# Kernel optimization log

Measured on AMD Instinct MI355X. Metric: run time of the kernel, lower is better.

The kernel has to match this reference:

```python
import jax, jax.numpy as jnp
import numpy as np

D_MODEL = 1024
N_HEADS = 16
HEAD_DIM = D_MODEL // N_HEADS
N_EXPERTS = 4
HIDDEN = 4 * D_MODEL
B, T = 1, 2048


def _apply_rope(x, sin, cos):
    # x: [..., D]; sin/cos broadcastable to [..., D/2]
    x1, x2 = x[..., ::2], x[..., 1::2]
    r1 = x1 * cos - x2 * sin
    r2 = x1 * sin + x2 * cos
    return jnp.stack((r1, r2), axis=-1).reshape(x.shape)


def setup_inputs() -> dict:
    key = jax.random.key(0)
    ks = jax.random.split(key, 16)
    s = 0.02
    d, E, Hd = D_MODEL, N_EXPERTS, HIDDEN
    return {
        "x": jax.random.normal(ks[0], (B, T, d), dtype=jnp.float32),
        "w_dw": jax.random.normal(ks[1], (d, 3), dtype=jnp.float32) * s,      # depthwise conv k=3
        "w_pw": jax.random.normal(ks[2], (d, d), dtype=jnp.float32) * s,      # pointwise conv [out,in]
        "w_qkv": jax.random.normal(ks[3], (3 * d, d), dtype=jnp.float32) * s,  # [out,in]
        "w_o": jax.random.normal(ks[4], (d, d), dtype=jnp.float32) * s,
        "w_gate": jax.random.normal(ks[5], (d, d), dtype=jnp.float32) * s,
        "b_gate": jnp.zeros((d,), dtype=jnp.float32),
        "ln_g": jnp.ones((d,), dtype=jnp.float32),
        "ln_b": jnp.zeros((d,), dtype=jnp.float32),
        "w_moe_gate": jax.random.normal(ks[6], (E, d), dtype=jnp.float32) * s,  # Linear no bias [out,in]
        "w1": jax.random.normal(ks[7], (E, Hd, d), dtype=jnp.float32) * s,
        "b1": jnp.zeros((E, Hd), dtype=jnp.float32),
        "w2": jax.random.normal(ks[8], (E, d, Hd), dtype=jnp.float32) * s,
        "b2": jnp.zeros((E, d), dtype=jnp.float32),
    }


def reference(x, w_dw, w_pw, w_qkv, w_o, w_gate, b_gate, ln_g, ln_b,
              w_moe_gate, w1, b1, w2, b2):
    Bv, Tv, d = x.shape
    H, Dh = N_HEADS, HEAD_DIM
    dt = x.dtype

    # --- causal conv mixer (depthwise k=3, causal left pad 2, then pointwise) ---
    xp = jnp.pad(x, ((0, 0), (2, 0), (0, 0)))
    y = (xp[:, 0:Tv] * w_dw[:, 0] + xp[:, 1:Tv + 1] * w_dw[:, 1]
         + xp[:, 2:Tv + 2] * w_dw[:, 2])
    y = jnp.einsum('btd,ed->bte', y, w_pw)
    x = x + y

    # --- qkv projection + split heads ---
    qkv = jnp.einsum('btd,ed->bte', x, w_qkv).reshape(Bv, Tv, 3, H, Dh)
    q, k, v = qkv[:, :, 0], qkv[:, :, 1], qkv[:, :, 2]

    # --- RoPE (head_dim even) ---
    inv_freq = 1.0 / (10000.0 ** (jnp.arange(0, Dh, 2, dtype=dt) / Dh))
    pos = jnp.arange(Tv, dtype=dt)
    theta = pos[:, None] * inv_freq[None, :]                 # [T, Dh/2]
    sin = jnp.sin(theta)[None, :, None, :]                   # [1,T,1,Dh/2]
    cos = jnp.cos(theta)[None, :, None, :]
    q = _apply_rope(q, sin, cos)
    k = _apply_rope(k, sin, cos)

    # --- linear attention via full kv outer-product cumsum ---
    q_phi = jax.nn.elu(q) + 1.0
    k_phi = jax.nn.elu(k) + 1.0
    kv = k_phi[..., :, None] * v[..., None, :]               # [B,T,H,D,D]
    kv_prefix = jnp.cumsum(kv, axis=1)
    k_prefix = jnp.cumsum(k_phi, axis=1)
    num = jnp.einsum('bthd,bthdm->bthm', q_phi, kv_prefix)
    denom = jnp.sum(q_phi * k_prefix, axis=-1, keepdims=True)
    attn = num / (denom + 1e-6)
    attn = attn.reshape(Bv, Tv, d)
    attn = jnp.einsum('btd,ed->bte', attn, w_o)

    # --- delta-gated residual (dropout = identity in eval) ---
    delta = x - jnp.concatenate([x[:, :1], x[:, :-1]], axis=1)
    gate = jax.nn.sigmoid(jnp.einsum('btd,ed->bte', delta, w_gate) + b_gate)
    x = x + gate * attn

    # --- LayerNorm + dense MoE FFN ---
    mu = jnp.mean(x, axis=-1, keepdims=True)
    var = jnp.mean((x - mu) ** 2, axis=-1, keepdims=True)
    h = (x - mu) / jnp.sqrt(var + 1e-5) * ln_g + ln_b

    gw = jax.nn.softmax(jnp.einsum('btd,ed->bte', h, w_moe_gate), axis=-1)  # [B,T,E]
    hid = jax.nn.silu(jnp.einsum('btd,efd->btef', h, w1) + b1)              # [B,T,E,Hd]
    eo = jnp.einsum('btef,edf->bted', hid, w2) + b2                          # [B,T,E,d]
    ffn = jnp.einsum('bte,bted->btd', gw, eo)
    return x + ffn
```

## Files before the change

### kernel.cpp

```cpp
#include <hip/hip_runtime.h>
#include <hip/hip_bf16.h>

#define TSEQ 2048
#define DM   1024
#define NHD  16
#define DHD  64
#define NEXP 4
#define HIDN 4096
#define NMOE (NEXP*HIDN)
#define CHK  128
#define NCHK (TSEQ/CHK)

typedef __attribute__((ext_vector_type(8))) short          bf16x8_v;
typedef __attribute__((ext_vector_type(4))) float          f32x4_v;
typedef __attribute__((ext_vector_type(4))) unsigned short us4_v;

__device__ __forceinline__ unsigned short bfbits(float f) {
  __hip_bfloat16 h = __float2bfloat16(f);
  return __builtin_bit_cast(unsigned short, h);
}
__device__ __forceinline__ float bf2f(unsigned short u) {
  return __uint_as_float(((unsigned)u) << 16);
}
__device__ __forceinline__ float wave_sum(float v) {
  #pragma unroll
  for (int o = 32; o; o >>= 1) v += __shfl_xor(v, o, 64);
  return v;
}
__device__ __forceinline__ void gl_lds16(const void* g, void* l) {
  __builtin_amdgcn_global_load_lds((const __attribute__((address_space(1))) void*)g,
                                   (__attribute__((address_space(3))) void*)l, 16, 0, 0);
}

__global__ __launch_bounds__(256) void cvt_bf16(const float* __restrict__ in,
                                                unsigned short* __restrict__ out, int n4) {
  int i = blockIdx.x * 256 + threadIdx.x;
  if (i >= n4) return;
  float4 v = ((const float4*)in)[i];
  us4_v o; o.x = bfbits(v.x); o.y = bfbits(v.y); o.z = bfbits(v.z); o.w = bfbits(v.w);
  ((us4_v*)out)[i] = o;
}

__global__ __launch_bounds__(256) void perm_w2(const float* __restrict__ in,
                                               unsigned short* __restrict__ out) {
  int i = blockIdx.x * 256 + threadIdx.x;
  int i4 = i * 4;
  int f = i4 & (HIDN - 1);
  int r = i4 >> 12;
  int e = r >> 10, dd = r & 1023;
  float4 v = *(const float4*)&in[(size_t)r * HIDN + f];
  us4_v o; o.x = bfbits(v.x); o.y = bfbits(v.y); o.z = bfbits(v.z); o.w = bfbits(v.w);
  *(us4_v*)&out[(size_t)dd * NMOE + e * HIDN + f] = o;
}

__global__ __launch_bounds__(256) void conv_dw(const float* __restrict__ x,
                                               const float* __restrict__ w_dw,
                                               unsigned short* __restrict__ y_bf) {
  int i = blockIdx.x * 256 + threadIdx.x;
  int c = i & (DM - 1);
  int t = i >> 10;
  float a = (t >= 2) ? x[i - 2 * DM] : 0.f;
  float b = (t >= 1) ? x[i - DM]     : 0.f;
  float d = x[i];
  float y = a * w_dw[c * 3] + b * w_dw[c * 3 + 1] + d * w_dw[c * 3 + 2];
  y_bf[i] = bfbits(y);
}

template <int EPI>
__global__ __launch_bounds__(256) void gemm_bt(
    const unsigned short* __restrict__ A,  const unsigned short* __restrict__ A2,
    const unsigned short* __restrict__ B,  const unsigned short* __restrict__ B2,
    float* __restrict__ Cf, float* __restrict__ Cf2,
    unsigned short* __restrict__ Cbf,
    const float* __restrict__ ex0, const float* __restrict__ ex1,
    int lda, int ldb, int K, int ldc, int kPerZ)
{
  if (EPI == 0) { if (blockIdx.z) { A = A2; B = B2; Cf = Cf2; } }
  if (EPI == 3) { int ko = blockIdx.z * kPerZ; A += ko; B += ko; }

  __shared__ unsigned short As[2][128][32];
  __shared__ unsigned short Bs[2][128][32];

  const int tid = threadIdx.x;
  const int m0 = blockIdx.x << 7, n0 = blockIdx.y << 7;
  const int sr = tid >> 2, sc = (tid & 3) << 3;
  const unsigned short* gA = A + (size_t)(m0 + sr) * lda + sc;
  const unsigned short* gB = B + (size_t)(n0 + sr) * ldb + sc;

  const int lane = tid & 63, wv = tid >> 6;
  const int wr = (wv >> 1) << 6, wc = (wv & 1) << 6;
  const int fr = lane & 15, fk = (lane >> 4) << 3, r4 = (lane >> 4) << 2;

  f32x4_v acc[4][4] = {};

  auto stage = [&](int k0, int b) {
    gl_lds16(gA + k0,                     &As[b][sr][sc]);
    gl_lds16(gA + k0 + (size_t)64 * lda,  &As[b][sr + 64][sc]);
    gl_lds16(gB + k0,                     &Bs[b][sr][sc]);
    gl_lds16(gB + k0 + (size_t)64 * ldb,  &Bs[b][sr + 64][sc]);
  };

  stage(0, 0);
  __syncthreads();
  int cur = 0;
  for (int k0 = 0; k0 < K; k0 += 32) {
    if (k0 + 32 < K) stage(k0 + 32, cur ^ 1);
    bf16x8_v af[4], bfm[4];
    #pragma unroll
    for (int m = 0; m < 4; m++) af[m]  = *(const bf16x8_v*)&As[cur][wr + m * 16 + fr][fk];
    #pragma unroll
    for (int n = 0; n < 4; n++) bfm[n] = *(const bf16x8_v*)&Bs[cur][wc + n * 16 + fr][fk];
    #pragma unroll
    for (int m = 0; m < 4; m++)
      #pragma unroll
      for (int n = 0; n < 4; n++)
        acc[m][n] = __builtin_amdgcn_mfma_f32_16x16x32_bf16(af[m], bfm[n], acc[m][n], 0, 0, 0);
    __syncthreads();
    cur ^= 1;
  }

  #pragma unroll
  for (int m = 0; m < 4; m++) {
    #pragma unroll
    for (int n = 0; n < 4; n++) {
      #pragma unroll
      for (int j = 0; j < 4; j++) {
        int gr = m0 + wr + m * 16 + r4 + j;
        int gc = n0 + wc + n * 16 + fr;
        float v = acc[m][n][j];
        size_t off = (size_t)gr * ldc + gc;
        if (EPI == 0) {
          Cf[off] = v;
        } else if (EPI == 1) {
          float s = v + ex0[off];
          Cf[off] = s; Cbf[off] = bfbits(s);
        } else if (EPI == 2) {
          float c2 = v + ex0[gc];
          float sl = c2 / (1.f + __expf(-c2));
          Cbf[off] = bfbits(sl * ex1[gr * 4 + (gc >> 12)]);
        } else {
          atomicAdd(&Cf[off], v);
        }
      }
    }
  }
}

__global__ __launch_bounds__(256) void rope_phi(const float* __restrict__ qkv,
                                                unsigned short* __restrict__ qphi,
                                                unsigned short* __restrict__ kphi,
                                                unsigned short* __restrict__ vout) {
  int idx = blockIdx.x * 256 + threadIdx.x;
  int i = idx & 31;
  int h = (idx >> 5) & 15;
  int t = idx >> 9;
  const float* row = qkv + (size_t)t * 3 * DM;
  int col = h * 64 + 2 * i;
  float q0 = row[col],          q1 = row[col + 1];
  float k0 = row[DM + col],     k1 = row[DM + col + 1];
  float v0 = row[2 * DM + col], v1 = row[2 * DM + col + 1];
  float invf = __expf(-(float)(2 * i) * (9.210340371976184f / 64.f));
  float th = (float)t * invf;
  float s, c;
  sincosf(th, &s, &c);
  float qr0 = q0 * c - q1 * s, qr1 = q0 * s + q1 * c;
  float kr0 = k0 * c - k1 * s, kr1 = k0 * s + k1 * c;
  size_t o = (size_t)t * DM + col;
  qphi[o]     = bfbits(qr0 > 0.f ? qr0 + 1.f : __expf(qr0));
  qphi[o + 1] = bfbits(qr1 > 0.f ? qr1 + 1.f : __expf(qr1));
  kphi[o]     = bfbits(kr0 > 0.f ? kr0 + 1.f : __expf(kr0));
  kphi[o + 1] = bfbits(kr1 > 0.f ? kr1 + 1.f : __expf(kr1));
  vout[o]     = bfbits(v0);
  vout[o + 1] = bfbits(v1);
}

__global__ __launch_bounds__(256) void kv_chunk(const unsigned short* __restrict__ kphi,
                                                const unsigned short* __restrict__ vbf,
                                                float* __restrict__ kvT,
                                                float* __restrict__ ksbuf) {
  int h = blockIdx.x & 15, c = blockIdx.x >> 4;
  __shared__ unsigned short Kt[64][136];
  __shared__ unsigned short Vt[64][136];
  int tid = threadIdx.x;
  int rr = tid >> 3, cc = (tid & 7) << 3;
  int t0 = c * CHK;
  #pragma unroll
  for (int g = 0; g < 4; g++) {
    int t = g * 32 + rr;
    bf16x8_v k8 = *(const bf16x8_v*)&kphi[(size_t)(t0 + t) * DM + h * 64 + cc];
    bf16x8_v v8 = *(const bf16x8_v*)&vbf [(size_t)(t0 + t) * DM + h * 64 + cc];
    #pragma unroll
    for (int j = 0; j < 8; j++) { Kt[cc + j][t] = (unsigned short)k8[j];
                                  Vt[cc + j][t] = (unsigned short)v8[j]; }
  }
  __syncthreads();
  int lane = tid & 63, wv = tid >> 6;
  int wr = (wv >> 1) << 5, wc = (wv & 1) << 5;
  int fr = lane & 15, fk = (lane >> 4) << 3, r4 = (lane >> 4) << 2;
  f32x4_v acc[2][2] = {};
  #pragma unroll
  for (int k0 = 0; k0 < 128; k0 += 32) {
    bf16x8_v a[2], b[2];
    #pragma unroll
    for (int m = 0; m < 2; m++) a[m] = *(const bf16x8_v*)&Kt[wr + m * 16 + fr][k0 + fk];
    #pragma unroll
    for (int n = 0; n < 2; n++) b[n] = *(const bf16x8_v*)&Vt[wc + n * 16 + fr][k0 + fk];
    #pragma unroll
    for (int m = 0; m < 2; m++)
      #pragma unroll
      for (int n = 0; n < 2; n++)
        acc[m][n] = __builtin_amdgcn_mfma_f32_16x16x32_bf16(a[m], b[n], acc[m][n], 0, 0, 0);
  }
  float* kvout = kvT + (size_t)(h * NCHK + c) * 4096;
  #pragma unroll
  for (int m = 0; m < 2; m++)
    #pragma unroll
    for (int n = 0; n < 2; n++)
      #pragma unroll
      for (int j = 0; j < 4; j++)
        kvout[(wc + n * 16 + fr) * 64 + (wr + m * 16 + r4 + j)] = acc[m][n][j];
  float s = 0.f;
  int d = tid >> 2, q = tid & 3;
  for (int i = 0; i < 32; i++) s += bf2f(Kt[d][q * 32 + i]);
  s += __shfl_xor(s, 1, 64); s += __shfl_xor(s, 2, 64);
  if (q == 0) ksbuf[(h * NCHK + c) * 64 + d] = s;
}

__global__ __launch_bounds__(256) void prefix_kv(const float* __restrict__ kvT,
                                                 const float* __restrict__ ksbuf,
                                                 unsigned short* __restrict__ sT,
                                                 float* __restrict__ kspre) {
  int idx = blockIdx.x * 256 + threadIdx.x;
  int h = idx >> 12, nd = idx & 4095;
  float s = 0.f;
  for (int c = 0; c < NCHK; c++) {
    size_t o = (size_t)(h * NCHK + c) * 4096 + nd;
    sT[o] = bfbits(s);
    s += kvT[o];
  }
  if (idx < NHD * 64) {
    float ks = 0.f;
    for (int c = 0; c < NCHK; c++) {
      int o = ((idx >> 6) * NCHK + c) * 64 + (idx & 63);
      kspre[o] = ks;
      ks += ksbuf[o];
    }
  }
}

__global__ __launch_bounds__(256) void attn_chunk(const unsigned short* __restrict__ qphi,
                                                  const unsigned short* __restrict__ kphi,
                                                  const unsigned short* __restrict__ vbf,
                                                  const unsigned short* __restrict__ sT,
                                                  const float* __restrict__ kspre,
                                                  float* __restrict__ num,
                                                  float* __restrict__ den) {
  int h = blockIdx.x & 15, c = blockIdx.x >> 4;
  __shared__ unsigned short Qs[128][72];
  __shared__ unsigned short Ks[128][72];
  __shared__ unsigned short Ms[128][200];
  __shared__ unsigned short Vt[64][200];
  __shared__ float ksL[64];
  int tid = threadIdx.x;
  int t0 = c * CHK;
  int rr = tid >> 3, cc = (tid & 7) << 3;
  #pragma unroll
  for (int g = 0; g < 4; g++) {
    int t = g * 32 + rr;
    bf16x8_v q8 = *(const bf16x8_v*)&qphi[(size_t)(t0 + t) * DM + h * 64 + cc];
    bf16x8_v k8 = *(const bf16x8_v*)&kphi[(size_t)(t0 + t) * DM + h * 64 + cc];
    bf16x8_v v8 = *(const bf16x8_v*)&vbf [(size_t)(t0 + t) * DM + h * 64 + cc];
    *(bf16x8_v*)&Qs[t][cc] = q8;
    *(bf16x8_v*)&Ks[t][cc] = k8;
    *(bf16x8_v*)&Ms[t][128 + cc] = q8;
    #pragma unroll
    for (int j = 0; j < 8; j++) Vt[cc + j][t] = (unsigned short)v8[j];
  }
  #pragma unroll
  for (int g = 0; g < 2; g++) {
    int e = (g * 256 + tid) * 8;
    bf16x8_v s8 = *(const bf16x8_v*)&sT[(size_t)(h * NCHK + c) * 4096 + e];
    *(bf16x8_v*)&Vt[e >> 6][128 + (e & 63)] = s8;
  }
  if (tid < 64) ksL[tid] = kspre[(h * NCHK + c) * 64 + tid];
  __syncthreads();

  int lane = tid & 63, wv = tid >> 6;
  int wr = (wv >> 1) << 6, wc = (wv & 1) << 6;
  int fr = lane & 15, fk = (lane >> 4) << 3, r4 = (lane >> 4) << 2;
  {
    f32x4_v acc[4][4] = {};
    #pragma unroll
    for (int k0 = 0; k0 < 64; k0 += 32) {
      bf16x8_v a[4], b[4];
      #pragma unroll
      for (int m = 0; m < 4; m++) a[m] = *(const bf16x8_v*)&Qs[wr + m * 16 + fr][k0 + fk];
      #pragma unroll
      for (int n = 0; n < 4; n++) b[n] = *(const bf16x8_v*)&Ks[wc + n * 16 + fr][k0 + fk];
      #pragma unroll
      for (int m = 0; m < 4; m++)
        #pragma unroll
        for (int n = 0; n < 4; n++)
          acc[m][n] = __builtin_amdgcn_mfma_f32_16x16x32_bf16(a[m], b[n], acc[m][n], 0, 0, 0);
    }
    #pragma unroll
    for (int m = 0; m < 4; m++)
      #pragma unroll
      for (int n = 0; n < 4; n++)
        #pragma unroll
        for (int j = 0; j < 4; j++) {
          int r = wr + m * 16 + r4 + j, col = wc + n * 16 + fr;
          Ms[r][col] = bfbits(col <= r ? acc[m][n][j] : 0.f);
        }
  }
  __syncthreads();
  {
    int dr = tid >> 1, half = tid & 1;
    float s = 0.f;
    for (int i = 0; i < 64; i++) s += bf2f(Ms[dr][half * 64 + i]);
    for (int i = 0; i < 32; i++) {
      int d = half * 32 + i;
      s += bf2f(Qs[dr][d]) * ksL[d];
    }
    s += __shfl_xor(s, 1, 64);
    if (!half) den[(size_t)(t0 + dr) * NHD + h] = s;
  }
  {
    int wc2 = (wv & 1) << 5;
    f32x4_v acc[4][2] = {};
    #pragma unroll
    for (int k0 = 0; k0 < 192; k0 += 32) {
      bf16x8_v a[4], b[2];
      #pragma unroll
      for (int m = 0; m < 4; m++) a[m] = *(const bf16x8_v*)&Ms[wr + m * 16 + fr][k0 + fk];
      #pragma unroll
      for (int n = 0; n < 2; n++) b[n] = *(const bf16x8_v*)&Vt[wc2 + n * 16 + fr][k0 + fk];
      #pragma unroll
      for (int m = 0; m < 4; m++)
        #pragma unroll
        for (int n = 0; n < 2; n++)
          acc[m][n] = __builtin_amdgcn_mfma_f32_16x16x32_bf16(a[m], b[n], acc[m][n], 0, 0, 0);
    }
    #pragma unroll
    for (int m = 0; m < 4; m++)
      #pragma unroll
      for (int n = 0; n < 2; n++)
        #pragma unroll
        for (int j = 0; j < 4; j++)
          num[(size_t)(t0 + wr + m * 16 + r4 + j) * DM + h * 64 + wc2 + n * 16 + fr]
              = acc[m][n][j];
  }
}

__global__ __launch_bounds__(256) void div_cvt(const float* __restrict__ attn_num,
                                               const float* __restrict__ denom,
                                               const float* __restrict__ x1,
                                               unsigned short* __restrict__ attn_bf,
                                               unsigned short* __restrict__ delta_bf) {
  int i = blockIdx.x * 256 + threadIdx.x;
  int i4 = i * 4;
  int t = i4 >> 10, c = i4 & 1023, h = c >> 6;
  float dn = 1.f / (denom[t * NHD + h] + 1e-6f);
  float4 nm = *(const float4*)&attn_num[i4];
  us4_v a; a.x = bfbits(nm.x * dn); a.y = bfbits(nm.y * dn);
           a.z = bfbits(nm.z * dn); a.w = bfbits(nm.w * dn);
  *(us4_v*)&attn_bf[i4] = a;
  float4 xv = *(const float4*)&x1[i4];
  float4 xp = t ? *(const float4*)&x1[i4 - DM] : xv;
  us4_v d; d.x = bfbits(xv.x - xp.x); d.y = bfbits(xv.y - xp.y);
           d.z = bfbits(xv.z - xp.z); d.w = bfbits(xv.w - xp.w);
  *(us4_v*)&delta_bf[i4] = d;
}

__global__ __launch_bounds__(256) void fuse_ln(const float* __restrict__ x1,
                                               const float* __restrict__ attn_o,
                                               const float* __restrict__ gate_lin,
                                               const float* __restrict__ b_gate,
                                               const float* __restrict__ ln_g,
                                               const float* __restrict__ ln_b,
                                               const float* __restrict__ w_moe,
                                               float* __restrict__ x2,
                                               unsigned short* __restrict__ h_bf,
                                               float* __restrict__ gw) {
  int t = blockIdx.x;
  int tid = threadIdx.x;
  __shared__ float hrow[DM];
  __shared__ float red[16];
  float vals[4], s = 0.f, s2 = 0.f;
  #pragma unroll
  for (int j = 0; j < 4; j++) {
    int c = tid + j * 256;
    size_t ix = (size_t)t * DM + c;
    float g = gate_lin[ix] + b_gate[c];
    float sig = 1.f / (1.f + __expf(-g));
    float xv = x1[ix] + sig * attn_o[ix];
    x2[ix] = xv; vals[j] = xv; s += xv; s2 += xv * xv;
  }
  s = wave_sum(s); s2 = wave_sum(s2);
  int wvi = tid >> 6, l = tid & 63;
  if (l == 0) { red[wvi] = s; red[4 + wvi] = s2; }
  __syncthreads();
  s  = red[0] + red[1] + red[2] + red[3];
  s2 = red[4] + red[5] + red[6] + red[7];
  float mu = s * (1.f / DM);
  float var = s2 * (1.f / DM) - mu * mu;
  float rstd = rsqrtf(var + 1e-5f);
  #pragma unroll
  for (int j = 0; j < 4; j++) {
    int c = tid + j * 256;
    size_t ix = (size_t)t * DM + c;
    float h = (vals[j] - mu) * rstd * ln_g[c] + ln_b[c];
    h_bf[ix] = bfbits(h); hrow[c] = h;
  }
  __syncthreads();
  float dot = 0.f;
  for (int i0 = l; i0 < DM; i0 += 64) dot += hrow[i0] * w_moe[wvi * DM + i0];
  dot = wave_sum(dot);
  if (l == 0) red[8 + wvi] = dot;
  __syncthreads();
  if (tid == 0) {
    float a0 = red[8], a1 = red[9], a2 = red[10], a3 = red[11];
    float mx = fmaxf(fmaxf(a0, a1), fmaxf(a2, a3));
    float e0 = __expf(a0 - mx), e1 = __expf(a1 - mx), e2 = __expf(a2 - mx), e3 = __expf(a3 - mx);
    float inv = 1.f / (e0 + e1 + e2 + e3);
    gw[t * 4 + 0] = e0 * inv; gw[t * 4 + 1] = e1 * inv;
    gw[t * 4 + 2] = e2 * inv; gw[t * 4 + 3] = e3 * inv;
  }
}

__global__ __launch_bounds__(256) void init_out(const float* __restrict__ x2,
                                                const float* __restrict__ gw,
                                                const float* __restrict__ b2,
                                                float* __restrict__ out) {
  int i = blockIdx.x * 256 + threadIdx.x;
  int i4 = i * 4;
  int t = i4 >> 10, c = i4 & 1023;
  const float* g = gw + t * 4;
  float4 o = *(const float4*)&x2[i4];
  #pragma unroll
  for (int e = 0; e < 4; e++) {
    float ge = g[e];
    float4 b = *(const float4*)&b2[e * DM + c];
    o.x += ge * b.x; o.y += ge * b.y; o.z += ge * b.z; o.w += ge * b.w;
  }
  *(float4*)&out[i4] = o;
}

extern "C" void kernel_launch(void* const* d_in, const int* in_sizes, int n_in,
                              void* d_out, int out_size, void* d_ws, size_t ws_size,
                              hipStream_t stream) {
  const float* x      = (const float*)d_in[0];
  const float* w_dw   = (const float*)d_in[1];
  const float* w_pw   = (const float*)d_in[2];
  const float* w_qkv  = (const float*)d_in[3];
  const float* w_o    = (const float*)d_in[4];
  const float* w_gate = (const float*)d_in[5];
  const float* b_gate = (const float*)d_in[6];
  const float* ln_g   = (const float*)d_in[7];
  const float* ln_b   = (const float*)d_in[8];
  const float* w_moe  = (const float*)d_in[9];
  const float* w1     = (const float*)d_in[10];
  const float* b1     = (const float*)d_in[11];
  const float* w2     = (const float*)d_in[12];
  const float* b2     = (const float*)d_in[13];
  float* out = (float*)d_out;

  char* ws = (char*)d_ws;
  size_t off = 0;
  auto alloc = [&](size_t bytes) -> char* {
    char* p = ws + off; off += (bytes + 255) & ~(size_t)255; return p;
  };
  unsigned short* w_pw_bf   = (unsigned short*)alloc((size_t)DM * DM * 2);
  unsigned short* w_qkv_bf  = (unsigned short*)alloc((size_t)3 * DM * DM * 2);
  unsigned short* w_o_bf    = (unsigned short*)alloc((size_t)DM * DM * 2);
  unsigned short* w_gate_bf = (unsigned short*)alloc((size_t)DM * DM * 2);
  unsigned short* w1_bf     = (unsigned short*)alloc((size_t)NMOE * DM * 2);
  unsigned short* w2c_bf    = (unsigned short*)alloc((size_t)DM * NMOE * 2);
  float*          x1        = (float*)alloc((size_t)TSEQ * DM * 4);
  unsigned short* x1_bf     = (unsigned short*)alloc((size_t)TSEQ * DM * 2);
  unsigned short* y_bf      = (unsigned short*)alloc((size_t)TSEQ * DM * 2);
  float*          denomb    = (float*)alloc((size_t)TSEQ * NHD * 4);
  float*          gwb       = (float*)alloc((size_t)TSEQ * NEXP * 4);
  float*          attn_o    = (float*)alloc((size_t)TSEQ * DM * 4);
  unsigned short* delta_bf  = (unsigned short*)alloc((size_t)TSEQ * DM * 2);
  float*          gate_lin  = (float*)alloc((size_t)TSEQ * DM * 4);
  float*          x2        = (float*)alloc((size_t)TSEQ * DM * 4);
  unsigned short* h_bf      = (unsigned short*)alloc((size_t)TSEQ * DM * 2);
  float*          kvT       = (float*)alloc((size_t)NHD * NCHK * 4096 * 4);
  unsigned short* sTb       = (unsigned short*)alloc((size_t)NHD * NCHK * 4096 * 2);
  float*          ksbuf     = (float*)alloc((size_t)NHD * NCHK * 64 * 4);
  float*          kspre     = (float*)alloc((size_t)NHD * NCHK * 64 * 4);
  char*           pool      = alloc((size_t)TSEQ * NMOE * 2);
  if (off > ws_size) return;

  float*          qkv      = (float*)pool;
  unsigned short* qphi     = (unsigned short*)(pool + (size_t)TSEQ * 3 * DM * 4);
  unsigned short* kphi     = qphi + (size_t)TSEQ * DM;
  unsigned short* vbf      = kphi + (size_t)TSEQ * DM;
  float*          attn_num = (float*)(vbf + (size_t)TSEQ * DM);
  unsigned short* attn_bf  = (unsigned short*)(attn_num + (size_t)TSEQ * DM);
  unsigned short* hids     = (unsigned short*)pool;

  cvt_bf16<<<1024,  256, 0, stream>>>(w_pw,   w_pw_bf,   DM * DM / 4);
  cvt_bf16<<<3072,  256, 0, stream>>>(w_qkv,  w_qkv_bf,  3 * DM * DM / 4);
  cvt_bf16<<<1024,  256, 0, stream>>>(w_o,    w_o_bf,    DM * DM / 4);
  cvt_bf16<<<1024,  256, 0, stream>>>(w_gate, w_gate_bf, DM * DM / 4);
  cvt_bf16<<<16384, 256, 0, stream>>>(w1,     w1_bf,     NMOE * DM / 4);
  perm_w2<<<16384, 256, 0, stream>>>(w2, w2c_bf);

  conv_dw<<<8192, 256, 0, stream>>>(x, w_dw, y_bf);
  gemm_bt<1><<<dim3(16, 8, 1), 256, 0, stream>>>(y_bf, nullptr, w_pw_bf, nullptr,
      x1, nullptr, x1_bf, x, nullptr, DM, DM, DM, DM, 0);

  gemm_bt<0><<<dim3(16, 24, 1), 256, 0, stream>>>(x1_bf, nullptr, w_qkv_bf, nullptr,
      qkv, nullptr, nullptr, nullptr, nullptr, DM, DM, DM, 3 * DM, 0);
  rope_phi<<<4096, 256, 0, stream>>>(qkv, qphi, kphi, vbf);

  kv_chunk<<<NHD * NCHK, 256, 0, stream>>>(kphi, vbf, kvT, ksbuf);
  prefix_kv<<<256, 256, 0, stream>>>(kvT, ksbuf, sTb, kspre);
  attn_chunk<<<NHD * NCHK, 256, 0, stream>>>(qphi, kphi, vbf, sTb, kspre,
                                             attn_num, denomb);
  div_cvt<<<2048, 256, 0, stream>>>(attn_num, denomb, x1, attn_bf, delta_bf);

  gemm_bt<0><<<dim3(16, 8, 2), 256, 0, stream>>>(attn_bf, delta_bf, w_o_bf, w_gate_bf,
      attn_o, gate_lin, nullptr, nullptr, nullptr, DM, DM, DM, DM, 0);

  fuse_ln<<<2048, 256, 0, stream>>>(x1, attn_o, gate_lin, b_gate, ln_g, ln_b, w_moe,
                                    x2, h_bf, gwb);

  init_out<<<2048, 256, 0, stream>>>(x2, gwb, b2, out);
  gemm_bt<2><<<dim3(16, 128, 1), 256, 0, stream>>>(h_bf, nullptr, w1_bf, nullptr,
      nullptr, nullptr, hids, b1, gwb, DM, DM, DM, NMOE, 0);
  gemm_bt<3><<<dim3(16, 8, 4), 256, 0, stream>>>(hids, nullptr, w2c_bf, nullptr,
      out, nullptr, nullptr, nullptr, nullptr, NMOE, NMOE, HIDN, DM, HIDN);
}
```

Baseline: 411.5 us.

## Add 256x256-tile GEMM kernel for the MoE FFN matmuls

Adds a new gemm256 kernel with 512 threads, 256x256 output tiles, BK=64, an XOR-swizzled LDS layout and a block-index swizzle for L2 locality. It replaces the 128x128 gemm_bt for the two large MoE GEMMs (w1 with the SiLU-gating epilogue, and w2 with split-K atomics, now split 8 ways instead of 4). The goal is more data reuse per block and fewer LDS bank conflicts on the dominant FLOP cost. The trade-off is higher register and LDS pressure (one block per CU), fewer blocks in the grid, and more atomic traffic from the wider split-K.

```diff
diff --git a/kernel.cpp b/kernel.cpp
--- a/kernel.cpp
+++ b/kernel.cpp
@@ -72,11 +72,10 @@
     const unsigned short* __restrict__ B,  const unsigned short* __restrict__ B2,
     float* __restrict__ Cf, float* __restrict__ Cf2,
     unsigned short* __restrict__ Cbf,
-    const float* __restrict__ ex0, const float* __restrict__ ex1,
-    int lda, int ldb, int K, int ldc, int kPerZ)
+    const float* __restrict__ ex0,
+    int lda, int ldb, int K, int ldc)
 {
   if (EPI == 0) { if (blockIdx.z) { A = A2; B = B2; Cf = Cf2; } }
-  if (EPI == 3) { int ko = blockIdx.z * kPerZ; A += ko; B += ko; }
 
   __shared__ unsigned short As[2][128][32];
   __shared__ unsigned short Bs[2][128][32];
@@ -131,19 +130,103 @@
         size_t off = (size_t)gr * ldc + gc;
         if (EPI == 0) {
           Cf[off] = v;
-        } else if (EPI == 1) {
+        } else {
           float s = v + ex0[off];
           Cf[off] = s; Cbf[off] = bfbits(s);
-        } else if (EPI == 2) {
-          float c2 = v + ex0[gc];
-          float sl = c2 / (1.f + __expf(-c2));
-          Cbf[off] = bfbits(sl * ex1[gr * 4 + (gc >> 12)]);
-        } else {
-          atomicAdd(&Cf[off], v);
         }
       }
     }
   }
+}
+
+template <int EPI>
+__global__ __launch_bounds__(512, 1) void gemm256(
+    const unsigned short* __restrict__ A, const unsigned short* __restrict__ B,
+    float* __restrict__ Cf, unsigned short* __restrict__ Cbf,
+    const float* __restrict__ ex0, const float* __restrict__ ex1,
+    int lda, int ldb, int K, int ldc, int kPerZ)
+{
+  if (EPI == 1) { int ko = blockIdx.z * kPerZ; A += ko; B += ko; K = kPerZ; }
+
+  __shared__ unsigned short As[2][256][64];
+  __shared__ unsigned short Bs[2][256][64];
+
+  int bidl = blockIdx.y * 8 + blockIdx.x;
+  int chunk = (gridDim.x * gridDim.y) >> 3;
+  int swz = (bidl & 7) * chunk + (bidl >> 3);
+  int m0 = (swz & 7) << 8, n0 = (swz >> 3) << 8;
+
+  const int tid = threadIdx.x;
+  const int srow = tid >> 3;
+  const int scol = (tid & 7) << 3;
+  const int scsw = scol ^ (((tid >> 5) & 1) << 4);
+  const unsigned short* gA = A + (size_t)(m0 + srow) * lda + scsw;
+  const unsigned short* gB = B + (size_t)(n0 + srow) * ldb + scsw;
+
+  auto stage = [&](int k0, int b) {
+    #pragma unroll
+    for (int i = 0; i < 4; i++)
+      gl_lds16(gA + (size_t)(i * 64) * lda + k0, &As[b][i * 64 + srow][scol]);
+    #pragma unroll
+    for (int i = 0; i < 4; i++)
+      gl_lds16(gB + (size_t)(i * 64) * ldb + k0, &Bs[b][i * 64 + srow][scol]);
+  };
+
+  const int lane = tid & 63, wv = tid >> 6;
+  const int wm = wv >> 2, wn = wv & 3;
+  const int fr = lane & 15;
+  const int fksw = ((lane >> 4) << 3) ^ (((fr >> 2) & 1) << 4);
+  const int r4 = (lane >> 4) << 2;
+
+  f32x4_v acc[8][4] = {};
+  stage(0, 0);
+  int cur = 0;
+  for (int k0 = 0; k0 < K; k0 += 64) {
+    if (k0 + 64 < K) {
+      stage(k0 + 64, cur ^ 1);
+      asm volatile("s_waitcnt vmcnt(8)" ::: "memory");
+    } else {
+      asm volatile("s_waitcnt vmcnt(0)" ::: "memory");
+    }
+    __builtin_amdgcn_s_barrier();
+    __builtin_amdgcn_sched_barrier(0);
+    #pragma unroll
+    for (int ks = 0; ks < 2; ks++) {
+      bf16x8_v a[8], bb[4];
+      #pragma unroll
+      for (int m = 0; m < 8; m++)
+        a[m] = *(const bf16x8_v*)&As[cur][wm * 128 + m * 16 + fr][ks * 32 + fksw];
+      #pragma unroll
+      for (int n = 0; n < 4; n++)
+        bb[n] = *(const bf16x8_v*)&Bs[cur][wn * 64 + n * 16 + fr][ks * 32 + fksw];
+      #pragma unroll
+      for (int m = 0; m < 8; m++)
+        #pragma unroll
+        for (int n = 0; n < 4; n++)
+          acc[m][n] = __builtin_amdgcn_mfma_f32_16x16x32_bf16(a[m], bb[n], acc[m][n], 0, 0, 0);
+    }
+    __builtin_amdgcn_sched_barrier(0);
+    __builtin_amdgcn_s_barrier();
+    cur ^= 1;
+  }
+
+  #pragma unroll
+  for (int m = 0; m < 8; m++)
+    #pragma unroll
+    for (int n = 0; n < 4; n++)
+      #pragma unroll
+      for (int j = 0; j < 4; j++) {
+        int grow = m0 + wm * 128 + m * 16 + r4 + j;
+        int gcol = n0 + wn * 64 + n * 16 + fr;
+        size_t off = (size_t)grow * ldc + gcol;
+        if (EPI == 0) {
+          float c2 = acc[m][n][j] + ex0[gcol];
+          float sl = c2 / (1.f + __expf(-c2));
+          Cbf[off] = bfbits(sl * ex1[grow * 4 + (gcol >> 12)]);
+        } else {
+          atomicAdd(&Cf[off], acc[m][n][j]);
+        }
+      }
 }
 
 __global__ __launch_bounds__(256) void rope_phi(const float* __restrict__ qkv,
@@ -510,10 +593,10 @@
 
   conv_dw<<<8192, 256, 0, stream>>>(x, w_dw, y_bf);
   gemm_bt<1><<<dim3(16, 8, 1), 256, 0, stream>>>(y_bf, nullptr, w_pw_bf, nullptr,
-      x1, nullptr, x1_bf, x, nullptr, DM, DM, DM, DM, 0);
+      x1, nullptr, x1_bf, x, DM, DM, DM, DM);
 
   gemm_bt<0><<<dim3(16, 24, 1), 256, 0, stream>>>(x1_bf, nullptr, w_qkv_bf, nullptr,
-      qkv, nullptr, nullptr, nullptr, nullptr, DM, DM, DM, 3 * DM, 0);
+      qkv, nullptr, nullptr, nullptr, DM, DM, DM, 3 * DM);
   rope_phi<<<4096, 256, 0, stream>>>(qkv, qphi, kphi, vbf);
 
   kv_chunk<<<NHD * NCHK, 256, 0, stream>>>(kphi, vbf, kvT, ksbuf);
@@ -523,14 +606,14 @@
   div_cvt<<<2048, 256, 0, stream>>>(attn_num, denomb, x1, attn_bf, delta_bf);
 
   gemm_bt<0><<<dim3(16, 8, 2), 256, 0, stream>>>(attn_bf, delta_bf, w_o_bf, w_gate_bf,
-      attn_o, gate_lin, nullptr, nullptr, nullptr, DM, DM, DM, DM, 0);
+      attn_o, gate_lin, nullptr, nullptr, DM, DM, DM, DM);
 
   fuse_ln<<<2048, 256, 0, stream>>>(x1, attn_o, gate_lin, b_gate, ln_g, ln_b, w_moe,
                                     x2, h_bf, gwb);
 
   init_out<<<2048, 256, 0, stream>>>(x2, gwb, b2, out);
-  gemm_bt<2><<<dim3(16, 128, 1), 256, 0, stream>>>(h_bf, nullptr, w1_bf, nullptr,
-      nullptr, nullptr, hids, b1, gwb, DM, DM, DM, NMOE, 0);
-  gemm_bt<3><<<dim3(16, 8, 4), 256, 0, stream>>>(hids, nullptr, w2c_bf, nullptr,
-      out, nullptr, nullptr, nullptr, nullptr, NMOE, NMOE, HIDN, DM, HIDN);
-}
+  gemm256<0><<<dim3(8, 64, 1), 512, 0, stream>>>(h_bf, w1_bf, nullptr, hids,
+      b1, gwb, DM, DM, DM, NMOE, 0);
+  gemm256<1><<<dim3(8, 4, 8), 512, 0, stream>>>(hids, w2c_bf, out, nullptr,
+      nullptr, nullptr, NMOE, NMOE, NMOE, DM, NMOE / 8);
+}
```

After: 418.1 us. No clear change (+1.6%).
